# Kernel optimization log

Hardware: AMD Instinct MI355X
Metric: run time of the kernel (lower is better)

## Reference

```python
import jax, jax.numpy as jnp
import numpy as np

N_NODES = 100000
N_EDGES = 600000
N_REL = 4
N_HEADS = 4
DIM = 128  # in_dim == out_dim (required by out = zeros_like(x) + index_add_ of out_dim msgs)
HEAD_DIM = DIM // N_HEADS
NEG_SLOPE = 0.2


def setup_inputs() -> dict:
    key = jax.random.key(0)
    k1, k2, k3, k4, k5 = jax.random.split(key, 5)
    x = jax.random.normal(k1, (N_NODES, DIM), dtype=jnp.float32)
    edge_index = jax.random.randint(k2, (2, N_EDGES), 0, N_NODES, dtype=jnp.int64)
    edge_types = jax.random.randint(k3, (N_EDGES,), 0, N_REL, dtype=jnp.int64)
    # per-relation linear weights, xavier-ish scale
    W = jax.random.normal(k4, (N_REL, DIM, DIM), dtype=jnp.float32) * (1.0 / np.sqrt(DIM))
    # attention vectors [R, H, 2*head_dim]
    attn = jax.random.normal(k5, (N_REL, N_HEADS, 2 * HEAD_DIM), dtype=jnp.float32) * 0.1
    return {"x": x, "edge_index": edge_index, "edge_types": edge_types, "W": W, "attn": attn}


def reference(x, edge_index, edge_types, W, attn):
    N = x.shape[0]
    R, H, twoD = attn.shape
    D = twoD // 2
    E = edge_types.shape[0]

    # per-relation linear transform: [R, N, H, D]
    x_rel = jnp.einsum('ni,rio->rno', x, W).reshape(R, N, H, D)

    src, dst = edge_index[0], edge_index[1]

    # gather per-edge features with the edge's relation
    src_feat = x_rel[edge_types, src]            # [E, H, D]
    dst_feat = x_rel[edge_types, dst]            # [E, H, D]
    a = attn[edge_types]                         # [E, H, 2D]

    # attention logits + LeakyReLU(0.2)
    cat = jnp.concatenate([src_feat, dst_feat], axis=-1)  # [E, H, 2D]
    alpha = jnp.sum(cat * a, axis=-1)                     # [E, H]
    alpha = jnp.where(alpha > 0, alpha, NEG_SLOPE * alpha)

    # segment softmax over edges sharing (relation, dst)
    seg = edge_types * N + dst                            # [E]
    S = R * N
    m = jax.ops.segment_max(alpha, seg, num_segments=S)   # [S, H]
    alpha_exp = jnp.exp(alpha - m[seg])
    denom = jax.ops.segment_sum(alpha_exp, seg, num_segments=S)
    w = alpha_exp / denom[seg]                            # [E, H]

    # weighted messages, scatter-add to dst
    msg = (src_feat * w[..., None]).reshape(E, H * D)     # [E, out_dim]
    out = jax.ops.segment_sum(msg, dst, num_segments=N)   # [N, out_dim]
    return out
```

## Files before the change

kernel.cpp:

```cpp
#include <hip/hip_runtime.h>
#include <hip/hip_bf16.h>
#include <stdint.h>

#define N_NODES 100000
#define N_EDGES 600000
#define N_REL 4
#define N_HEADS 4
#define DIM 128
#define HEAD_DIM 32
#define NEG_SLOPE 0.2f

typedef unsigned int uint;
typedef unsigned short ushort;
typedef __attribute__((ext_vector_type(8))) short bf16x8;
typedef __attribute__((ext_vector_type(4))) float f32x4;

__device__ __forceinline__ float bf2f(ushort u) { return __uint_as_float(((uint)u) << 16); }
__device__ __forceinline__ float lo2f(uint u) { return __uint_as_float(u << 16); }
__device__ __forceinline__ float hi2f(uint u) { return __uint_as_float(u & 0xffff0000u); }
__device__ __forceinline__ ushort f2bf(float f) {
    uint u = __float_as_uint(f);
    uint r = (u + 0x7fffu + ((u >> 16) & 1u)) >> 16;
    return (ushort)r;
}
__device__ __forceinline__ float lrelu(float v) { return v > 0.f ? v : NEG_SLOPE * v; }

__device__ __forceinline__ int bf16_plaus(ushort u) {
    int ex = (u >> 7) & 0xFF;
    return (ex >= 100 && ex <= 140) ? 1 : 0;
}
__device__ __forceinline__ int vote_f32(const ushort* p) {
    int lane = threadIdx.x & 63;
    unsigned long long b0 = __ballot(bf16_plaus(p[2 * lane]) != 0);
    unsigned long long b1 = __ballot(bf16_plaus(p[2 * (lane + 64)]) != 0);
    return (__popcll(b0) + __popcll(b1)) < 64;
}
__device__ __forceinline__ int vote_i64(const int* p) {
    int lane = threadIdx.x & 63;
    unsigned long long b0 = __ballot(p[2 * lane + 1] != 0);
    unsigned long long b1 = __ballot(p[2 * (lane + 64) + 1] != 0);
    return (__popcll(b0) + __popcll(b1)) < 8;
}

__global__ __launch_bounds__(256) void k_prep(
    const void* __restrict__ xv, const void* __restrict__ Wv,
    const void* __restrict__ av,
    ushort* __restrict__ x_bf, ushort* __restrict__ Wt_g,
    ushort* __restrict__ at_g)
{
    __shared__ ushort wt[128][136];
    const int tid = threadIdx.x;

    if (blockIdx.x < N_REL) {
        const int r = blockIdx.x;
        const int wf = vote_f32((const ushort*)Wv);
        const int af = vote_f32((const ushort*)av);

        if (wf) {
            const float4* Wg = (const float4*)((const float*)Wv + (size_t)r * DIM * DIM);
            for (int it = 0; it < 16; ++it) {
                int idx = tid + it * 256;
                int k = idx >> 5, n4 = (idx & 31) * 4;
                float4 v = Wg[idx];
                wt[n4 + 0][k] = f2bf(v.x);
                wt[n4 + 1][k] = f2bf(v.y);
                wt[n4 + 2][k] = f2bf(v.z);
                wt[n4 + 3][k] = f2bf(v.w);
            }
        } else {
            const ushort* Wg = (const ushort*)Wv + (size_t)r * DIM * DIM;
            for (int it = 0; it < 16; ++it) {
                int idx = tid + it * 256;
                int k = idx >> 5, n4 = (idx & 31) * 4;
                const ushort* p = Wg + (size_t)k * DIM + n4;
                wt[n4 + 0][k] = p[0];
                wt[n4 + 1][k] = p[1];
                wt[n4 + 2][k] = p[2];
                wt[n4 + 3][k] = p[3];
            }
        }
        __syncthreads();

        for (int it = 0; it < 9; ++it) {
            int idx = tid + it * 256;
            if (idx < 2176) {
                int row = idx / 17, c8 = (idx % 17) * 8;
                *(uint4*)(Wt_g + ((size_t)r * 128 + row) * 136 + c8) = *(const uint4*)&wt[row][c8];
            }
        }
        for (int it = 0; it < 9; ++it) {
            int idx = tid + it * 256;
            if (idx < 16 * 136) {
                int n = idx / 136, k = idx % 136;
                int h = n & 3, sd = (n >> 2) & 1;
                float v = 0.f;
                if (n < 8 && k < 128) {
                    int d = k - h * 32;
                    if (d >= 0 && d < 32) {
                        size_t ai = ((size_t)(r * N_HEADS + h)) * 64 + (size_t)sd * 32 + d;
                        v = af ? ((const float*)av)[ai] : bf2f(((const ushort*)av)[ai]);
                    }
                }
                at_g[((size_t)r * 16 + n) * 136 + k] = f2bf(v);
            }
        }
    } else {
        const int xf = vote_f32((const ushort*)xv);
        int t = (blockIdx.x - N_REL) * 256 + tid;
        if (t >= N_NODES * DIM / 8) return;
        if (xf) {
            const float4* p = (const float4*)xv + (size_t)t * 2;
            float4 f0 = p[0], f1 = p[1];
            uint4 o;
            o.x = (uint)f2bf(f0.x) | ((uint)f2bf(f0.y) << 16);
            o.y = (uint)f2bf(f0.z) | ((uint)f2bf(f0.w) << 16);
            o.z = (uint)f2bf(f1.x) | ((uint)f2bf(f1.y) << 16);
            o.w = (uint)f2bf(f1.z) | ((uint)f2bf(f1.w) << 16);
            ((uint4*)x_bf)[t] = o;
        } else {
            ((uint4*)x_bf)[t] = ((const uint4*)xv)[t];
        }
    }
}

__global__ __launch_bounds__(256) void k_gemm_mfma(
    const ushort* __restrict__ x_bf, const ushort* __restrict__ Wt_g,
    const ushort* __restrict__ at_g,
    ushort* __restrict__ x_rel, float* __restrict__ sTab)
{
    __shared__ ushort wt[128][136];
    __shared__ ushort at[16][136];

    const int tid = threadIdx.x;
    const int wave = tid >> 6, lane = tid & 63;
    const int quad = lane >> 4, l16 = lane & 15;
    const int r = blockIdx.x & 3;
    const int n0 = (blockIdx.x >> 2) * 128;

    {
        const uint4* src  = (const uint4*)(Wt_g + (size_t)r * 128 * 136);
        const uint4* srcA = (const uint4*)(at_g + (size_t)r * 16 * 136);
        uint4* dstL = (uint4*)&wt[0][0];
        uint4* dstA = (uint4*)&at[0][0];
#pragma unroll
        for (int it = 0; it < 10; ++it) {
            int idx = tid + it * 256;
            if (idx < 2176) dstL[idx] = src[idx];
            else if (idx < 2448) dstA[idx - 2176] = srcA[idx - 2176];
        }
    }

    const int rowA0 = n0 + wave * 32 + l16;
    const int rowA1 = rowA0 + 16;
    const size_t rA0 = (size_t)min(rowA0, N_NODES - 1) * DIM;
    const size_t rA1 = (size_t)min(rowA1, N_NODES - 1) * DIM;

    __syncthreads();

    f32x4 acc[2][8];
#pragma unroll
    for (int rt = 0; rt < 2; ++rt)
#pragma unroll
        for (int ct = 0; ct < 8; ++ct) acc[rt][ct] = (f32x4){0.f, 0.f, 0.f, 0.f};

#pragma unroll
    for (int q = 0; q < 4; ++q) {
        const int kb = q * 32 + quad * 8;
        bf16x8 a0 = *(const bf16x8*)(x_bf + rA0 + kb);
        bf16x8 a1 = *(const bf16x8*)(x_bf + rA1 + kb);
#pragma unroll
        for (int ct = 0; ct < 8; ++ct) {
            bf16x8 b = *(const bf16x8*)&wt[ct * 16 + l16][kb];
            acc[0][ct] = __builtin_amdgcn_mfma_f32_16x16x32_bf16(a0, b, acc[0][ct], 0, 0, 0);
            acc[1][ct] = __builtin_amdgcn_mfma_f32_16x16x32_bf16(a1, b, acc[1][ct], 0, 0, 0);
        }
    }
    __syncthreads();

    {
        ushort* rp = &wt[0][0];
#pragma unroll
        for (int rt = 0; rt < 2; ++rt) {
            int rowb = wave * 32 + rt * 16 + quad * 4;
#pragma unroll
            for (int ct = 0; ct < 8; ++ct) {
                int col = ct * 16 + l16;
#pragma unroll
                for (int reg = 0; reg < 4; ++reg)
                    rp[(rowb + reg) * 136 + col] = f2bf(acc[rt][ct][reg]);
            }
        }
    }
    __syncthreads();

    {
        const ushort* rp = &wt[0][0];
        f32x4 sacc[2];
        sacc[0] = (f32x4){0.f, 0.f, 0.f, 0.f};
        sacc[1] = (f32x4){0.f, 0.f, 0.f, 0.f};
#pragma unroll
        for (int q = 0; q < 4; ++q) {
            const int kb = q * 32 + quad * 8;
            bf16x8 a0 = *(const bf16x8*)(rp + (wave * 32 + l16) * 136 + kb);
            bf16x8 a1 = *(const bf16x8*)(rp + (wave * 32 + 16 + l16) * 136 + kb);
            bf16x8 bat = *(const bf16x8*)&at[l16][kb];
            sacc[0] = __builtin_amdgcn_mfma_f32_16x16x32_bf16(a0, bat, sacc[0], 0, 0, 0);
            sacc[1] = __builtin_amdgcn_mfma_f32_16x16x32_bf16(a1, bat, sacc[1], 0, 0, 0);
        }
        if (l16 < 8) {
#pragma unroll
            for (int rt = 0; rt < 2; ++rt) {
#pragma unroll
                for (int reg = 0; reg < 4; ++reg) {
                    int node = n0 + wave * 32 + rt * 16 + quad * 4 + reg;
                    if (node < N_NODES)
                        sTab[((size_t)r * N_NODES + node) * 8 + l16] = sacc[rt][reg];
                }
            }
        }
    }

    {
        const ushort* rp = &wt[0][0];
        const size_t rbase = (size_t)r * N_NODES * DIM;
#pragma unroll
        for (int p = 0; p < 8; ++p) {
            int row = p * 16 + (tid >> 4);
            int chunk = tid & 15;
            int node = n0 + row;
            if (node < N_NODES) {
                uint4 v = *(const uint4*)(rp + row * 136 + chunk * 8);
                *(uint4*)(x_rel + rbase + (size_t)node * DIM + chunk * 8) = v;
            }
        }
    }
}

__global__ __launch_bounds__(256) void k_hist2(
    const int* __restrict__ ei, uint* __restrict__ deg)
{
    const int i64e = vote_i64(ei);
    int e = blockIdx.x * 256 + threadIdx.x;
    if (e >= N_EDGES) return;
    int d = i64e ? ei[2 * (N_EDGES + e)] : ei[N_EDGES + e];
    atomicAdd(&deg[d], 1u);
}

__global__ __launch_bounds__(256) void k_scan1(
    const uint* __restrict__ deg, uint* __restrict__ excl, uint* __restrict__ bsum)
{
    __shared__ uint tmp[256];
    int i = blockIdx.x * 256 + threadIdx.x;
    uint v = (i < N_NODES) ? deg[i] : 0u;
    tmp[threadIdx.x] = v;
    __syncthreads();
    for (int off = 1; off < 256; off <<= 1) {
        uint t = (threadIdx.x >= off) ? tmp[threadIdx.x - off] : 0u;
        __syncthreads();
        tmp[threadIdx.x] += t;
        __syncthreads();
    }
    if (i < N_NODES) excl[i] = tmp[threadIdx.x] - v;
    if (threadIdx.x == 255) bsum[blockIdx.x] = tmp[255];
}

__global__ __launch_bounds__(256) void k_scan23(
    const uint* __restrict__ excl, const uint* __restrict__ bsum,
    uint* __restrict__ start, uint* __restrict__ cursor, int nblocks)
{
    __shared__ uint off_s;
    if (threadIdx.x < 64) {
        int lane = threadIdx.x;
        uint acc = 0;
        for (int j = lane; j < blockIdx.x; j += 64) acc += bsum[j];
        for (int o = 32; o; o >>= 1) acc += __shfl_down(acc, o);
        if (lane == 0) off_s = acc;
    }
    __syncthreads();
    uint off = off_s;
    int i = blockIdx.x * 256 + threadIdx.x;
    if (i >= N_NODES) return;
    uint s = excl[i] + off;
    start[i] = s;
    cursor[i] = s;
}

__global__ __launch_bounds__(256) void k_fill_y(
    const int* __restrict__ ei, const int* __restrict__ et,
    const float* __restrict__ sTab,
    uint* __restrict__ cursor, uint* __restrict__ csrPack,
    float4* __restrict__ yTab)
{
    const int i64e = vote_i64(ei);
    const int i64t = vote_i64(et);
    int e = blockIdx.x * 256 + threadIdx.x;
    if (e >= N_EDGES) return;
    int s = i64e ? ei[2 * e] : ei[e];
    int d = i64e ? ei[2 * (N_EDGES + e)] : ei[N_EDGES + e];
    int r = i64t ? et[2 * e] : et[e];
    float4 a = *(const float4*)(sTab + ((size_t)r * N_NODES + s) * 8);
    float4 b = *(const float4*)(sTab + ((size_t)r * N_NODES + d) * 8 + 4);
    float4 y;
    y.x = __expf(lrelu(a.x + b.x));
    y.y = __expf(lrelu(a.y + b.y));
    y.z = __expf(lrelu(a.z + b.z));
    y.w = __expf(lrelu(a.w + b.w));
    uint pos = atomicAdd(&cursor[d], 1u);
    csrPack[pos] = (uint)s | ((uint)r << 27);
    yTab[pos] = y;
}

__global__ __launch_bounds__(256) void k_norm(
    const uint* __restrict__ start, const uint* __restrict__ deg,
    const uint* __restrict__ csrPack, const float4* __restrict__ yTab,
    float4* __restrict__ dTab)
{
    int dst = blockIdx.x * 256 + threadIdx.x;
    if (dst >= N_NODES) return;
    const uint st = start[dst];
    const uint dg = deg[dst];

    float4 s0 = {0.f, 0.f, 0.f, 0.f}, s1 = s0, s2 = s0, s3 = s0;

#define NACC(J, VLD) { \
    uint re = pk##J >> 27; \
    float vm = (VLD) ? 1.f : 0.f; \
    float yx = y##J.x * vm, yy = y##J.y * vm, yz = y##J.z * vm, yw = y##J.w * vm; \
    s0.x += (re == 0) ? yx : 0.f; s0.y += (re == 0) ? yy : 0.f; \
    s0.z += (re == 0) ? yz : 0.f; s0.w += (re == 0) ? yw : 0.f; \
    s1.x += (re == 1) ? yx : 0.f; s1.y += (re == 1) ? yy : 0.f; \
    s1.z += (re == 1) ? yz : 0.f; s1.w += (re == 1) ? yw : 0.f; \
    s2.x += (re == 2) ? yx : 0.f; s2.y += (re == 2) ? yy : 0.f; \
    s2.z += (re == 2) ? yz : 0.f; s2.w += (re == 2) ? yw : 0.f; \
    s3.x += (re == 3) ? yx : 0.f; s3.y += (re == 3) ? yy : 0.f; \
    s3.z += (re == 3) ? yz : 0.f; s3.w += (re == 3) ? yw : 0.f; \
}
    if (dg != 0u) {
        const uint last = st + dg - 1u;
        for (uint e0 = 0; e0 < dg; e0 += 4) {
            uint i0 = st + e0;
            uint i1 = (i0 + 1u <= last) ? i0 + 1u : last;
            uint i2 = (i0 + 2u <= last) ? i0 + 2u : last;
            uint i3 = (i0 + 3u <= last) ? i0 + 3u : last;
            uint pk0 = csrPack[i0], pk1 = csrPack[i1];
            uint pk2 = csrPack[i2], pk3 = csrPack[i3];
            float4 y0 = yTab[i0], y1 = yTab[i1], y2 = yTab[i2], y3 = yTab[i3];
            NACC(0, 1)
            NACC(1, e0 + 1u < dg)
            NACC(2, e0 + 2u < dg)
            NACC(3, e0 + 3u < dg)
        }
    }
#undef NACC

    float4 r0, r1, r2, r3;
    r0.x = s0.x > 0.f ? 1.f / s0.x : 0.f; r0.y = s0.y > 0.f ? 1.f / s0.y : 0.f;
    r0.z = s0.z > 0.f ? 1.f / s0.z : 0.f; r0.w = s0.w > 0.f ? 1.f / s0.w : 0.f;
    r1.x = s1.x > 0.f ? 1.f / s1.x : 0.f; r1.y = s1.y > 0.f ? 1.f / s1.y : 0.f;
    r1.z = s1.z > 0.f ? 1.f / s1.z : 0.f; r1.w = s1.w > 0.f ? 1.f / s1.w : 0.f;
    r2.x = s2.x > 0.f ? 1.f / s2.x : 0.f; r2.y = s2.y > 0.f ? 1.f / s2.y : 0.f;
    r2.z = s2.z > 0.f ? 1.f / s2.z : 0.f; r2.w = s2.w > 0.f ? 1.f / s2.w : 0.f;
    r3.x = s3.x > 0.f ? 1.f / s3.x : 0.f; r3.y = s3.y > 0.f ? 1.f / s3.y : 0.f;
    r3.z = s3.z > 0.f ? 1.f / s3.z : 0.f; r3.w = s3.w > 0.f ? 1.f / s3.w : 0.f;
    dTab[(size_t)0 * N_NODES + dst] = r0;
    dTab[(size_t)1 * N_NODES + dst] = r1;
    dTab[(size_t)2 * N_NODES + dst] = r2;
    dTab[(size_t)3 * N_NODES + dst] = r3;
}

__global__ __launch_bounds__(256) void k_gather5(
    const uint* __restrict__ start, const uint* __restrict__ deg,
    const uint* __restrict__ csrPack, const float* __restrict__ dTab,
    const float* __restrict__ yTab,
    const uint* __restrict__ x_rel_u, float* __restrict__ out)
{
    const int wv = threadIdx.x >> 6;
    const int dst = blockIdx.x * 4 + wv;
    if (dst >= N_NODES) return;
    const int lane = threadIdx.x & 63;
    const int h = lane >> 4;

    const uint st = start[dst];
    const uint dg = deg[dst];

    float rs0 = dTab[((size_t)0 * N_NODES + dst) * 4 + h];
    float rs1 = dTab[((size_t)1 * N_NODES + dst) * 4 + h];
    float rs2 = dTab[((size_t)2 * N_NODES + dst) * 4 + h];
    float rs3 = dTab[((size_t)3 * N_NODES + dst) * 4 + h];

    float a0 = 0.f, a1 = 0.f;

#define GACC(J, VLD) { \
    uint re = pk##J >> 27, sx = pk##J & 0x07FFFFFFu; (void)sx; \
    float rs = (re < 2) ? (re == 0 ? rs0 : rs1) : (re == 2 ? rs2 : rs3); \
    float mw = (VLD) ? y##J * rs : 0.f; \
    a0 = fmaf(mw, lo2f(u##J), a0); a1 = fmaf(mw, hi2f(u##J), a1); \
}
    if (dg != 0u) {
        const uint last = st + dg - 1u;
        for (uint e0 = 0; e0 < dg; e0 += 8) {
            uint i0 = st + e0;
            uint i1 = (i0 + 1u <= last) ? i0 + 1u : last;
            uint i2 = (i0 + 2u <= last) ? i0 + 2u : last;
            uint i3 = (i0 + 3u <= last) ? i0 + 3u : last;
            uint i4 = (i0 + 4u <= last) ? i0 + 4u : last;
            uint i5 = (i0 + 5u <= last) ? i0 + 5u : last;
            uint i6 = (i0 + 6u <= last) ? i0 + 6u : last;
            uint i7 = (i0 + 7u <= last) ? i0 + 7u : last;
            uint pk0 = csrPack[i0], pk1 = csrPack[i1];
            uint pk2 = csrPack[i2], pk3 = csrPack[i3];
            uint pk4 = csrPack[i4], pk5 = csrPack[i5];
            uint pk6 = csrPack[i6], pk7 = csrPack[i7];
            float y0 = yTab[(size_t)i0 * 4 + h], y1 = yTab[(size_t)i1 * 4 + h];
            float y2 = yTab[(size_t)i2 * 4 + h], y3 = yTab[(size_t)i3 * 4 + h];
            float y4 = yTab[(size_t)i4 * 4 + h], y5 = yTab[(size_t)i5 * 4 + h];
            float y6 = yTab[(size_t)i6 * 4 + h], y7 = yTab[(size_t)i7 * 4 + h];
            uint u0 = x_rel_u[((size_t)(pk0 >> 27) * N_NODES + (pk0 & 0x07FFFFFFu)) * 64 + lane];
            uint u1 = x_rel_u[((size_t)(pk1 >> 27) * N_NODES + (pk1 & 0x07FFFFFFu)) * 64 + lane];
            uint u2 = x_rel_u[((size_t)(pk2 >> 27) * N_NODES + (pk2 & 0x07FFFFFFu)) * 64 + lane];
            uint u3 = x_rel_u[((size_t)(pk3 >> 27) * N_NODES + (pk3 & 0x07FFFFFFu)) * 64 + lane];
            uint u4 = x_rel_u[((size_t)(pk4 >> 27) * N_NODES + (pk4 & 0x07FFFFFFu)) * 64 + lane];
            uint u5 = x_rel_u[((size_t)(pk5 >> 27) * N_NODES + (pk5 & 0x07FFFFFFu)) * 64 + lane];
            uint u6 = x_rel_u[((size_t)(pk6 >> 27) * N_NODES + (pk6 & 0x07FFFFFFu)) * 64 + lane];
            uint u7 = x_rel_u[((size_t)(pk7 >> 27) * N_NODES + (pk7 & 0x07FFFFFFu)) * 64 + lane];
            GACC(0, 1)
            GACC(1, e0 + 1u < dg)
            GACC(2, e0 + 2u < dg)
            GACC(3, e0 + 3u < dg)
            GACC(4, e0 + 4u < dg)
            GACC(5, e0 + 5u < dg)
            GACC(6, e0 + 6u < dg)
            GACC(7, e0 + 7u < dg)
        }
    }
#undef GACC

    float2 o; o.x = a0; o.y = a1;
    *(float2*)(out + (size_t)dst * DIM + lane * 2) = o;
}

extern "C" void kernel_launch(void* const* d_in, const int* in_sizes, int n_in,
                              void* d_out, int out_size, void* d_ws, size_t ws_size,
                              hipStream_t stream) {
    const void* x    = d_in[0];
    const int*  ei   = (const int*)d_in[1];
    const int*  et   = (const int*)d_in[2];
    const void* W    = d_in[3];
    const void* attn = d_in[4];
    float* out = (float*)d_out;

    char* ws = (char*)d_ws;
    float*  sTab    = (float*)(ws + 7200256);
    ushort* x_rel   = (ushort*)(ws + 20000256);
    uint*   deg     = (uint*)(ws + 122400256);
    uint*   excl    = (uint*)(ws + 122800256);
    uint*   bsum    = (uint*)(ws + 123200256);
    uint*   startA  = (uint*)(ws + 123202304);
    uint*   cursor  = (uint*)(ws + 123602304);
    uint*   csrPack = (uint*)(ws + 124002304);
    ushort* x_bf    = (ushort*)(ws + 126402304);
    ushort* Wt_g    = (ushort*)(ws + 122800256);
    ushort* at_g    = (ushort*)(ws + 123202304);
    float4* dTab    = (float4*)(ws + 126402304);
    float4* yTab    = (float4*)(ws + 132802304);

    const int NBLK = (N_NODES + 255) / 256;

    hipMemsetAsync(deg, 0, 400000, stream);

    k_prep<<<N_REL + (N_NODES * DIM / 8 + 255) / 256, 256, 0, stream>>>(
        x, W, attn, x_bf, Wt_g, at_g);
    k_hist2<<<(N_EDGES + 255) / 256, 256, 0, stream>>>(ei, deg);

    k_gemm_mfma<<<((N_NODES + 127) / 128) * N_REL, 256, 0, stream>>>(x_bf, Wt_g, at_g,
                                                                     x_rel, sTab);

    k_scan1<<<NBLK, 256, 0, stream>>>(deg, excl, bsum);
    k_scan23<<<NBLK, 256, 0, stream>>>(excl, bsum, startA, cursor, NBLK);
    k_fill_y<<<(N_EDGES + 255) / 256, 256, 0, stream>>>(ei, et, sTab, cursor,
                                                        csrPack, yTab);
    k_norm<<<NBLK, 256, 0, stream>>>(startA, deg, csrPack, yTab, dTab);
    k_gather5<<<(N_NODES + 3) / 4, 256, 0, stream>>>(startA, deg, csrPack,
                                                     (const float*)dTab,
                                                     (const float*)yTab,
                                                     (const uint*)x_rel, out);
}
```

Baseline: 286.6 us.

## Fuse histogram into prep, scan into GEMM, and normalization into gather

Folds the degree histogram into the prep kernel as extra blocks, with each thread now counting four edges through vectorized loads. The first scan pass runs as extra blocks of the GEMM launch. The separate normalization kernel is removed: the gather kernel now computes per-relation softmax denominators itself with a first pass over each node's edges, so the dTab round trip is gone. This cuts three kernel launches and some global traffic, at the cost of reading csrPack and yTab twice inside the gather and adding redundant per-lane work.

```diff
diff --git a/kernel.cpp b/kernel.cpp
--- a/kernel.cpp
+++ b/kernel.cpp
@@ -42,11 +42,16 @@
     return (__popcll(b0) + __popcll(b1)) < 8;
 }
 
+#define XBLKS ((N_NODES * DIM / 8 + 255) / 256)
+#define HBLKS ((N_EDGES / 4 + 255) / 256)
+#define GBLKS (((N_NODES + 127) / 128) * N_REL)
+#define NBLKS ((N_NODES + 255) / 256)
+
 __global__ __launch_bounds__(256) void k_prep(
     const void* __restrict__ xv, const void* __restrict__ Wv,
-    const void* __restrict__ av,
+    const void* __restrict__ av, const int* __restrict__ ei,
     ushort* __restrict__ x_bf, ushort* __restrict__ Wt_g,
-    ushort* __restrict__ at_g)
+    ushort* __restrict__ at_g, uint* __restrict__ deg)
 {
     __shared__ ushort wt[128][136];
     const int tid = threadIdx.x;
@@ -104,7 +109,7 @@
                 at_g[((size_t)r * 16 + n) * 136 + k] = f2bf(v);
             }
         }
-    } else {
+    } else if (blockIdx.x < N_REL + XBLKS) {
         const int xf = vote_f32((const ushort*)xv);
         int t = (blockIdx.x - N_REL) * 256 + tid;
         if (t >= N_NODES * DIM / 8) return;
@@ -120,18 +125,56 @@
         } else {
             ((uint4*)x_bf)[t] = ((const uint4*)xv)[t];
         }
-    }
-}
-
-__global__ __launch_bounds__(256) void k_gemm_mfma(
+    } else {
+        const int i64e = vote_i64(ei);
+        int e0 = ((blockIdx.x - N_REL - XBLKS) * 256 + tid) * 4;
+        if (e0 >= N_EDGES) return;
+        int d0, d1, d2, d3;
+        if (i64e) {
+            int4 v0 = *(const int4*)&ei[2 * (N_EDGES + e0)];
+            int4 v1 = *(const int4*)&ei[2 * (N_EDGES + e0) + 4];
+            d0 = v0.x; d1 = v0.z; d2 = v1.x; d3 = v1.z;
+        } else {
+            int4 v = *(const int4*)&ei[N_EDGES + e0];
+            d0 = v.x; d1 = v.y; d2 = v.z; d3 = v.w;
+        }
+        atomicAdd(&deg[d0], 1u);
+        atomicAdd(&deg[d1], 1u);
+        atomicAdd(&deg[d2], 1u);
+        atomicAdd(&deg[d3], 1u);
+    }
+}
+
+__global__ __launch_bounds__(256) void k_gemm_scan(
     const ushort* __restrict__ x_bf, const ushort* __restrict__ Wt_g,
     const ushort* __restrict__ at_g,
-    ushort* __restrict__ x_rel, float* __restrict__ sTab)
+    ushort* __restrict__ x_rel, float* __restrict__ sTab,
+    const uint* __restrict__ deg, uint* __restrict__ excl,
+    uint* __restrict__ bsum)
 {
     __shared__ ushort wt[128][136];
     __shared__ ushort at[16][136];
 
     const int tid = threadIdx.x;
+
+    if (blockIdx.x >= GBLKS) {
+        uint* tmp = (uint*)&wt[0][0];
+        int sb = blockIdx.x - GBLKS;
+        int i = sb * 256 + tid;
+        uint v = (i < N_NODES) ? deg[i] : 0u;
+        tmp[tid] = v;
+        __syncthreads();
+        for (int off = 1; off < 256; off <<= 1) {
+            uint t = (tid >= off) ? tmp[tid - off] : 0u;
+            __syncthreads();
+            tmp[tid] += t;
+            __syncthreads();
+        }
+        if (i < N_NODES) excl[i] = tmp[tid] - v;
+        if (tid == 255) bsum[sb] = tmp[255];
+        return;
+    }
+
     const int wave = tid >> 6, lane = tid & 63;
     const int quad = lane >> 4, l16 = lane & 15;
     const int r = blockIdx.x & 3;
@@ -234,34 +277,6 @@
             }
         }
     }
-}
-
-__global__ __launch_bounds__(256) void k_hist2(
-    const int* __restrict__ ei, uint* __restrict__ deg)
-{
-    const int i64e = vote_i64(ei);
-    int e = blockIdx.x * 256 + threadIdx.x;
-    if (e >= N_EDGES) return;
-    int d = i64e ? ei[2 * (N_EDGES + e)] : ei[N_EDGES + e];
-    atomicAdd(&deg[d], 1u);
-}
-
-__global__ __launch_bounds__(256) void k_scan1(
-    const uint* __restrict__ deg, uint* __restrict__ excl, uint* __restrict__ bsum)
-{
-    __shared__ uint tmp[256];
-    int i = blockIdx.x * 256 + threadIdx.x;
-    uint v = (i < N_NODES) ? deg[i] : 0u;
-    tmp[threadIdx.x] = v;
-    __syncthreads();
-    for (int off = 1; off < 256; off <<= 1) {
-        uint t = (threadIdx.x >= off) ? tmp[threadIdx.x - off] : 0u;
-        __syncthreads();
-        tmp[threadIdx.x] += t;
-        __syncthreads();
-    }
-    if (i < N_NODES) excl[i] = tmp[threadIdx.x] - v;
-    if (threadIdx.x == 255) bsum[blockIdx.x] = tmp[255];
 }
 
 __global__ __launch_bounds__(256) void k_scan23(
@@ -310,33 +325,34 @@
     yTab[pos] = y;
 }
 
-__global__ __launch_bounds__(256) void k_norm(
+__global__ __launch_bounds__(256) void k_gather6(
     const uint* __restrict__ start, const uint* __restrict__ deg,
-    const uint* __restrict__ csrPack, const float4* __restrict__ yTab,
-    float4* __restrict__ dTab)
+    const uint* __restrict__ csrPack, const float* __restrict__ yTab,
+    const uint* __restrict__ x_rel_u, float* __restrict__ out)
 {
-    int dst = blockIdx.x * 256 + threadIdx.x;
+    const int wv = threadIdx.x >> 6;
+    const int dst = blockIdx.x * 4 + wv;
     if (dst >= N_NODES) return;
+    const int lane = threadIdx.x & 63;
+    const int h = lane >> 4;
+
     const uint st = start[dst];
     const uint dg = deg[dst];
 
-    float4 s0 = {0.f, 0.f, 0.f, 0.f}, s1 = s0, s2 = s0, s3 = s0;
-
-#define NACC(J, VLD) { \
-    uint re = pk##J >> 27; \
-    float vm = (VLD) ? 1.f : 0.f; \
-    float yx = y##J.x * vm, yy = y##J.y * vm, yz = y##J.z * vm, yw = y##J.w * vm; \
-    s0.x += (re == 0) ? yx : 0.f; s0.y += (re == 0) ? yy : 0.f; \
-    s0.z += (re == 0) ? yz : 0.f; s0.w += (re == 0) ? yw : 0.f; \
-    s1.x += (re == 1) ? yx : 0.f; s1.y += (re == 1) ? yy : 0.f; \
-    s1.z += (re == 1) ? yz : 0.f; s1.w += (re == 1) ? yw : 0.f; \
-    s2.x += (re == 2) ? yx : 0.f; s2.y += (re == 2) ? yy : 0.f; \
-    s2.z += (re == 2) ? yz : 0.f; s2.w += (re == 2) ? yw : 0.f; \
-    s3.x += (re == 3) ? yx : 0.f; s3.y += (re == 3) ? yy : 0.f; \
-    s3.z += (re == 3) ? yz : 0.f; s3.w += (re == 3) ? yw : 0.f; \
-}
+    float a0 = 0.f, a1 = 0.f;
+
     if (dg != 0u) {
         const uint last = st + dg - 1u;
+
+        float ds0 = 0.f, ds1 = 0.f, ds2 = 0.f, ds3 = 0.f;
+#define DACC(J, VLD) { \
+    uint re = pk##J >> 27; \
+    float yv = (VLD) ? y##J : 0.f; \
+    ds0 += (re == 0) ? yv : 0.f; \
+    ds1 += (re == 1) ? yv : 0.f; \
+    ds2 += (re == 2) ? yv : 0.f; \
+    ds3 += (re == 3) ? yv : 0.f; \
+}
         for (uint e0 = 0; e0 < dg; e0 += 4) {
             uint i0 = st + e0;
             uint i1 = (i0 + 1u <= last) ? i0 + 1u : last;
@@ -344,60 +360,25 @@
             uint i3 = (i0 + 3u <= last) ? i0 + 3u : last;
             uint pk0 = csrPack[i0], pk1 = csrPack[i1];
             uint pk2 = csrPack[i2], pk3 = csrPack[i3];
-            float4 y0 = yTab[i0], y1 = yTab[i1], y2 = yTab[i2], y3 = yTab[i3];
-            NACC(0, 1)
-            NACC(1, e0 + 1u < dg)
-            NACC(2, e0 + 2u < dg)
-            NACC(3, e0 + 3u < dg)
-        }
-    }
-#undef NACC
-
-    float4 r0, r1, r2, r3;
-    r0.x = s0.x > 0.f ? 1.f / s0.x : 0.f; r0.y = s0.y > 0.f ? 1.f / s0.y : 0.f;
-    r0.z = s0.z > 0.f ? 1.f / s0.z : 0.f; r0.w = s0.w > 0.f ? 1.f / s0.w : 0.f;
-    r1.x = s1.x > 0.f ? 1.f / s1.x : 0.f; r1.y = s1.y > 0.f ? 1.f / s1.y : 0.f;
-    r1.z = s1.z > 0.f ? 1.f / s1.z : 0.f; r1.w = s1.w > 0.f ? 1.f / s1.w : 0.f;
-    r2.x = s2.x > 0.f ? 1.f / s2.x : 0.f; r2.y = s2.y > 0.f ? 1.f / s2.y : 0.f;
-    r2.z = s2.z > 0.f ? 1.f / s2.z : 0.f; r2.w = s2.w > 0.f ? 1.f / s2.w : 0.f;
-    r3.x = s3.x > 0.f ? 1.f / s3.x : 0.f; r3.y = s3.y > 0.f ? 1.f / s3.y : 0.f;
-    r3.z = s3.z > 0.f ? 1.f / s3.z : 0.f; r3.w = s3.w > 0.f ? 1.f / s3.w : 0.f;
-    dTab[(size_t)0 * N_NODES + dst] = r0;
-    dTab[(size_t)1 * N_NODES + dst] = r1;
-    dTab[(size_t)2 * N_NODES + dst] = r2;
-    dTab[(size_t)3 * N_NODES + dst] = r3;
-}
-
-__global__ __launch_bounds__(256) void k_gather5(
-    const uint* __restrict__ start, const uint* __restrict__ deg,
-    const uint* __restrict__ csrPack, const float* __restrict__ dTab,
-    const float* __restrict__ yTab,
-    const uint* __restrict__ x_rel_u, float* __restrict__ out)
-{
-    const int wv = threadIdx.x >> 6;
-    const int dst = blockIdx.x * 4 + wv;
-    if (dst >= N_NODES) return;
-    const int lane = threadIdx.x & 63;
-    const int h = lane >> 4;
-
-    const uint st = start[dst];
-    const uint dg = deg[dst];
-
-    float rs0 = dTab[((size_t)0 * N_NODES + dst) * 4 + h];
-    float rs1 = dTab[((size_t)1 * N_NODES + dst) * 4 + h];
-    float rs2 = dTab[((size_t)2 * N_NODES + dst) * 4 + h];
-    float rs3 = dTab[((size_t)3 * N_NODES + dst) * 4 + h];
-
-    float a0 = 0.f, a1 = 0.f;
+            float y0 = yTab[(size_t)i0 * 4 + h], y1 = yTab[(size_t)i1 * 4 + h];
+            float y2 = yTab[(size_t)i2 * 4 + h], y3 = yTab[(size_t)i3 * 4 + h];
+            DACC(0, 1)
+            DACC(1, e0 + 1u < dg)
+            DACC(2, e0 + 2u < dg)
+            DACC(3, e0 + 3u < dg)
+        }
+#undef DACC
+        float rs0 = (ds0 > 0.f) ? 1.f / ds0 : 0.f;
+        float rs1 = (ds1 > 0.f) ? 1.f / ds1 : 0.f;
+        float rs2 = (ds2 > 0.f) ? 1.f / ds2 : 0.f;
+        float rs3 = (ds3 > 0.f) ? 1.f / ds3 : 0.f;
 
 #define GACC(J, VLD) { \
-    uint re = pk##J >> 27, sx = pk##J & 0x07FFFFFFu; (void)sx; \
+    uint re = pk##J >> 27; \
     float rs = (re < 2) ? (re == 0 ? rs0 : rs1) : (re == 2 ? rs2 : rs3); \
     float mw = (VLD) ? y##J * rs : 0.f; \
     a0 = fmaf(mw, lo2f(u##J), a0); a1 = fmaf(mw, hi2f(u##J), a1); \
 }
-    if (dg != 0u) {
-        const uint last = st + dg - 1u;
         for (uint e0 = 0; e0 < dg; e0 += 8) {
             uint i0 = st + e0;
             uint i1 = (i0 + 1u <= last) ? i0 + 1u : last;
@@ -432,8 +413,8 @@
             GACC(6, e0 + 6u < dg)
             GACC(7, e0 + 7u < dg)
         }
-    }
 #undef GACC
+    }
 
     float2 o; o.x = a0; o.y = a1;
     *(float2*)(out + (size_t)dst * DIM + lane * 2) = o;
@@ -450,6 +431,8 @@
     float* out = (float*)d_out;
 
     char* ws = (char*)d_ws;
+    ushort* Wt_g    = (ushort*)(ws + 0);
+    ushort* at_g    = (ushort*)(ws + 139264);
     float*  sTab    = (float*)(ws + 7200256);
     ushort* x_rel   = (ushort*)(ws + 20000256);
     uint*   deg     = (uint*)(ws + 122400256);
@@ -459,29 +442,20 @@
     uint*   cursor  = (uint*)(ws + 123602304);
     uint*   csrPack = (uint*)(ws + 124002304);
     ushort* x_bf    = (ushort*)(ws + 126402304);
-    ushort* Wt_g    = (ushort*)(ws + 122800256);
-    ushort* at_g    = (ushort*)(ws + 123202304);
-    float4* dTab    = (float4*)(ws + 126402304);
-    float4* yTab    = (float4*)(ws + 132802304);
-
-    const int NBLK = (N_NODES + 255) / 256;
+    float4* yTab    = (float4*)(ws + 126402304);
 
     hipMemsetAsync(deg, 0, 400000, stream);
 
-    k_prep<<<N_REL + (N_NODES * DIM / 8 + 255) / 256, 256, 0, stream>>>(
-        x, W, attn, x_bf, Wt_g, at_g);
-    k_hist2<<<(N_EDGES + 255) / 256, 256, 0, stream>>>(ei, deg);
-
-    k_gemm_mfma<<<((N_NODES + 127) / 128) * N_REL, 256, 0, stream>>>(x_bf, Wt_g, at_g,
-                                                                     x_rel, sTab);
-
-    k_scan1<<<NBLK, 256, 0, stream>>>(deg, excl, bsum);
-    k_scan23<<<NBLK, 256, 0, stream>>>(excl, bsum, startA, cursor, NBLK);
+    k_prep<<<N_REL + XBLKS + HBLKS, 256, 0, stream>>>(
+        x, W, attn, ei, x_bf, Wt_g, at_g, deg);
+
+    k_gemm_scan<<<GBLKS + NBLKS, 256, 0, stream>>>(x_bf, Wt_g, at_g,
+                                                   x_rel, sTab, deg, excl, bsum);
+
+    k_scan23<<<NBLKS, 256, 0, stream>>>(excl, bsum, startA, cursor, NBLKS);
     k_fill_y<<<(N_EDGES + 255) / 256, 256, 0, stream>>>(ei, et, sTab, cursor,
                                                         csrPack, yTab);
-    k_norm<<<NBLK, 256, 0, stream>>>(startA, deg, csrPack, yTab, dTab);
-    k_gather5<<<(N_NODES + 3) / 4, 256, 0, stream>>>(startA, deg, csrPack,
-                                                     (const float*)dTab,
+    k_gather6<<<(N_NODES + 3) / 4, 256, 0, stream>>>(startA, deg, csrPack,
                                                      (const float*)yTab,
                                                      (const uint*)x_rel, out);
 }
```

Measured after the change: 296.4 us. +3.4%, slower.
